# Optimization experiments

Measured on AMD Instinct MI355X. Metric: run time of the kernel, lower is better.

## Reference

```python
import jax, jax.numpy as jnp
import numpy as np
import itertools

G = 80          # voxel grid side
N = 200000      # active voxels
A, B = 64, 128  # in/out channels
K = 27          # 3x3x3 kernel offsets
EPS = 1e-5


def _build_kernel_map():
    rng = np.random.default_rng(0)
    flat = rng.choice(G ** 3, size=N, replace=False)
    coords = np.stack(np.unravel_index(flat, (G, G, G)), axis=1).astype(np.int64)  # [N,3]
    lookup = np.full(G ** 3, -1, dtype=np.int64)
    lookup[flat] = np.arange(N)
    gidx = np.full((K, N), N, dtype=np.int32)  # pad with dummy row N
    sidx = np.full((K, N), N, dtype=np.int32)
    for k, off in enumerate(itertools.product([-1, 0, 1], repeat=3)):
        nb = coords + np.asarray(off)
        valid = np.all((nb >= 0) & (nb < G), axis=1)
        i_all = np.nonzero(valid)[0]
        nbf = np.ravel_multi_index(nb[valid].T, (G, G, G))
        j = lookup[nbf]
        m = j >= 0
        i, j = i_all[m], j[m]
        e = len(i)
        gidx[k, :e] = j   # gather neighbor features
        sidx[k, :e] = i   # scatter to output voxel
    return jnp.asarray(gidx), jnp.asarray(sidx)


def setup_inputs() -> dict:
    key = jax.random.key(0)
    ks = jax.random.split(key, 8)
    gidx, sidx = _build_kernel_map()
    return {
        "feats": jax.random.normal(ks[0], (N, A), jnp.float32),
        "w1": jax.random.normal(ks[1], (K, A, B), jnp.float32) * (1.0 / np.sqrt(K * A)),
        "w2": jax.random.normal(ks[2], (K, B, B), jnp.float32) * (1.0 / np.sqrt(K * B)),
        "w_nin": jax.random.normal(ks[3], (A, B), jnp.float32) * (1.0 / np.sqrt(A)),
        "bn1_gamma": jnp.ones((A,), jnp.float32),
        "bn1_beta": jnp.zeros((A,), jnp.float32),
        "bn2_gamma": jnp.ones((B,), jnp.float32),
        "bn2_beta": jnp.zeros((B,), jnp.float32),
        "gidx": gidx,
        "sidx": sidx,
    }


def _bn(x, gamma, beta):
    # MinkowskiBatchNorm: per-channel stats over all active voxels (training mode)
    mean = jnp.mean(x, axis=0)
    var = jnp.var(x, axis=0)
    return (x - mean) * jax.lax.rsqrt(var + EPS) * gamma + beta


def _sparse_conv(feats, w, gidx, sidx):
    # Minkowski sparse conv: for each kernel offset k, gather neighbor feats,
    # apply W[k], scatter-add to output voxel. Dummy row N absorbs padding.
    fp = jnp.concatenate([feats, jnp.zeros((1, feats.shape[1]), feats.dtype)], axis=0)
    out = jnp.zeros((N + 1, w.shape[-1]), feats.dtype)
    for k in range(w.shape[0]):  # fixed 27 offsets
        out = out.at[sidx[k]].add(fp[gidx[k]] @ w[k])
    return out[:N]


def reference(feats, w1, w2, w_nin, bn1_gamma, bn1_beta, bn2_gamma, bn2_beta, gidx, sidx):
    # resblock: BN(a) -> conv3(a->b) -> BN(b) -> conv3(b->b); skip via 1x1 conv (a!=b)
    h = _bn(feats, bn1_gamma, bn1_beta)
    h = _sparse_conv(h, w1, gidx, sidx)
    h = _bn(h, bn2_gamma, bn2_beta)
    residual = _sparse_conv(h, w2, gidx, sidx)
    skip = feats @ w_nin  # kernel_size=1 conv == per-voxel linear
    return skip + residual
```

## Files before the change

kernel.cpp:

```cpp
#include <hip/hip_runtime.h>

#define N_VOX 200000
#define NPAD_INV (27 * N_VOX + 128)
#define EPS_BN 1e-5f

typedef __bf16 bf16x8 __attribute__((ext_vector_type(8)));
typedef float f32x4 __attribute__((ext_vector_type(4)));

__device__ __forceinline__ float bf2f(unsigned short u) {
    union { float f; unsigned int i; } x; x.i = ((unsigned int)u) << 16; return x.f;
}
__device__ __forceinline__ unsigned short f2bf(float f) {
    union { float f; unsigned int i; } x; x.f = f;
    unsigned int r = x.i + 0x7fffu + ((x.i >> 16) & 1u);
    return (unsigned short)(r >> 16);
}

#define ASYNC16(gsrc, ldst)                                                             \
    __builtin_amdgcn_global_load_lds(                                                   \
        (const __attribute__((address_space(1))) void*)(gsrc),                          \
        (__attribute__((address_space(3))) void*)(ldst), 16, 0, 0)

__global__ void fill_inv_kernel(int* __restrict__ inv) {
    for (int i = blockIdx.x * 256 + threadIdx.x; i < NPAD_INV; i += gridDim.x * 256)
        inv[i] = N_VOX;
}

__global__ void build_inv_kernel(const int* __restrict__ sidx, const int* __restrict__ gidx,
                                 int* __restrict__ inv) {
    int k = blockIdx.y;
    int p = blockIdx.x * 256 + threadIdx.x;
    if (p < N_VOX) {
        int s = sidx[k * N_VOX + p];
        if (s < N_VOX) inv[k * N_VOX + s] = gidx[k * N_VOX + p];
    }
}

__global__ void tr_w1_kernel(const float* __restrict__ w, unsigned short* __restrict__ wt) {
    int k = blockIdx.y; int idx = blockIdx.x * 256 + threadIdx.x;
    int a = idx >> 7, b = idx & 127;
    wt[k * 8192 + b * 64 + a] = f2bf(w[k * 8192 + idx]);
}
__global__ void tr_w2_kernel(const float* __restrict__ w, unsigned short* __restrict__ wt) {
    int k = blockIdx.y; int idx = blockIdx.x * 256 + threadIdx.x;
    int a = idx >> 7, b = idx & 127;
    wt[k * 16384 + b * 128 + a] = f2bf(w[k * 16384 + idx]);
}
__global__ void tr_wn_kernel(const float* __restrict__ w, unsigned short* __restrict__ wt) {
    int idx = blockIdx.x * 256 + threadIdx.x;
    int a = idx >> 7, b = idx & 127;
    wt[b * 64 + a] = f2bf(w[idx]);
}

__global__ void stats1_kernel(const float* __restrict__ feats,
                              float* __restrict__ sum, float* __restrict__ sq) {
    int t = threadIdx.x; int c = t & 63; int rg = t >> 6;
    float s = 0.f, q = 0.f;
    for (int row = blockIdx.x * 4 + rg; row < N_VOX; row += gridDim.x * 4) {
        float x = feats[(size_t)row * 64 + c];
        s += x; q += x * x;
    }
    __shared__ float red[8][64];
    red[rg][c] = s; red[4 + rg][c] = q;
    __syncthreads();
    if (t < 64) atomicAdd(&sum[t], red[0][t] + red[1][t] + red[2][t] + red[3][t]);
    else if (t < 128) { int cc = t - 64; atomicAdd(&sq[cc], red[4][cc] + red[5][cc] + red[6][cc] + red[7][cc]); }
}

__global__ void stats2_kernel(const unsigned short* __restrict__ h1b,
                              float* __restrict__ sum, float* __restrict__ sq) {
    int t = threadIdx.x; int c = t & 127; int rg = t >> 7;
    float s = 0.f, q = 0.f;
    for (int row = blockIdx.x * 2 + rg; row < N_VOX; row += gridDim.x * 2) {
        float x = bf2f(h1b[(size_t)row * 128 + c]);
        s += x; q += x * x;
    }
    __shared__ float red[4][128];
    red[rg][c] = s; red[2 + rg][c] = q;
    __syncthreads();
    if (t < 128) atomicAdd(&sum[t], red[0][t] + red[1][t]);
    else { int cc = t - 128; atomicAdd(&sq[cc], red[2][cc] + red[3][cc]); }
}

__global__ void norm1_kernel(const float* __restrict__ feats, const float* __restrict__ ssum,
                             const float* __restrict__ ssq, const float* __restrict__ gamma,
                             const float* __restrict__ beta, unsigned short* __restrict__ fA,
                             unsigned short* __restrict__ fRaw) {
    __shared__ float sc[64], sh[64];
    int t = threadIdx.x;
    if (t < 64) {
        float mean = ssum[t] * (1.0f / N_VOX);
        float var  = ssq[t] * (1.0f / N_VOX) - mean * mean;
        float s    = gamma[t] * rsqrtf(var + EPS_BN);
        sc[t] = s; sh[t] = beta[t] - mean * s;
    }
    __syncthreads();
    const int total = N_VOX * 64 / 8;
    int i = blockIdx.x * 256 + t;
    if (i >= total) return;
    int cb = (i * 8) & 63;
    const float4* src = (const float4*)(feats + (size_t)i * 8);
    float4 f0 = src[0], f1 = src[1];
    float fv[8] = {f0.x, f0.y, f0.z, f0.w, f1.x, f1.y, f1.z, f1.w};
    union { uint4 q; unsigned short u[8]; } a, r;
#pragma unroll
    for (int j = 0; j < 8; j++) {
        a.u[j] = f2bf(fv[j] * sc[cb + j] + sh[cb + j]);
        r.u[j] = f2bf(fv[j]);
    }
    *(uint4*)(fA + (size_t)i * 8) = a.q;
    *(uint4*)(fRaw + (size_t)i * 8) = r.q;
}

__global__ void norm2_kernel(unsigned short* __restrict__ h1b, const float* __restrict__ ssum,
                             const float* __restrict__ ssq, const float* __restrict__ gamma,
                             const float* __restrict__ beta) {
    __shared__ float sc[128], sh[128];
    int t = threadIdx.x;
    if (t < 128) {
        float mean = ssum[t] * (1.0f / N_VOX);
        float var  = ssq[t] * (1.0f / N_VOX) - mean * mean;
        float s    = gamma[t] * rsqrtf(var + EPS_BN);
        sc[t] = s; sh[t] = beta[t] - mean * s;
    }
    __syncthreads();
    const int total = N_VOX * 128 / 8;
    int i = blockIdx.x * 256 + t;
    if (i >= total) return;
    int cb = (i * 8) & 127;
    union { uint4 q; unsigned short u[8]; } v;
    v.q = *(const uint4*)(h1b + (size_t)i * 8);
#pragma unroll
    for (int j = 0; j < 8; j++) v.u[j] = f2bf(bf2f(v.u[j]) * sc[cb + j] + sh[cb + j]);
    *(uint4*)(h1b + (size_t)i * 8) = v.q;
}

__global__ __launch_bounds__(256) void conv1_kernel(
    const unsigned short* __restrict__ fA, const unsigned short* __restrict__ w1t,
    const int* __restrict__ inv, const unsigned short* __restrict__ zp,
    unsigned short* __restrict__ h1b) {
    __shared__ __align__(16) unsigned short sA[128 * 64];
    __shared__ __align__(16) unsigned short sB[128 * 64];
    const int t = threadIdx.x, lane = t & 63, w = t >> 6;
    const int v0 = blockIdx.x * 128;
    const int srow = w * 32;
    const int lrow = lane >> 3;
    const int lcol = (lane & 7) * 8;
    const int scol = lcol ^ (lrow * 8);
    const int m0 = (w & 1) * 64, n0 = (w >> 1) * 64;
    const int l16 = lane & 15, quad = lane >> 4;
    const int xs = l16 & 7;
    f32x4 acc[4][4] = {};

    for (int k = 0; k < 27; k++) {
#pragma unroll
        for (int q = 0; q < 4; q++) {
            int rt = srow + q * 8 + lrow;
            int g = inv[k * N_VOX + v0 + rt];
            const unsigned short* asrc = (g < N_VOX) ? (fA + (size_t)g * 64 + scol) : (zp + scol);
            ASYNC16(asrc, &sA[(srow + q * 8) * 64]);
            const unsigned short* bsrc = w1t + k * 8192 + rt * 64 + scol;
            ASYNC16(bsrc, &sB[(srow + q * 8) * 64]);
        }
        __syncthreads();
#pragma unroll
        for (int ks = 0; ks < 2; ks++) {
            const int cs = ((ks * 4 + quad) ^ xs) * 8;
            bf16x8 af[4], bfr[4];
#pragma unroll
            for (int mi = 0; mi < 4; mi++)
                af[mi] = *(const bf16x8*)&sA[(m0 + mi * 16 + l16) * 64 + cs];
#pragma unroll
            for (int ni = 0; ni < 4; ni++)
                bfr[ni] = *(const bf16x8*)&sB[(n0 + ni * 16 + l16) * 64 + cs];
#pragma unroll
            for (int mi = 0; mi < 4; mi++)
#pragma unroll
                for (int ni = 0; ni < 4; ni++)
                    acc[mi][ni] = __builtin_amdgcn_mfma_f32_16x16x32_bf16(af[mi], bfr[ni], acc[mi][ni], 0, 0, 0);
        }
        __syncthreads();
    }
#pragma unroll
    for (int mi = 0; mi < 4; mi++)
#pragma unroll
        for (int r = 0; r < 4; r++) {
            int v = v0 + m0 + mi * 16 + quad * 4 + r;
            if (v < N_VOX) {
#pragma unroll
                for (int ni = 0; ni < 4; ni++)
                    h1b[(size_t)v * 128 + n0 + ni * 16 + l16] = f2bf(acc[mi][ni][r]);
            }
        }
}

__global__ __launch_bounds__(256) void conv2_kernel(
    const unsigned short* __restrict__ h1n, const unsigned short* __restrict__ fRaw,
    const unsigned short* __restrict__ w2t, const unsigned short* __restrict__ w_nint,
    const int* __restrict__ inv, const unsigned short* __restrict__ zp,
    float* __restrict__ out) {
    __shared__ __align__(16) unsigned short sA[128 * 64];
    __shared__ __align__(16) unsigned short sB[128 * 64];
    const int t = threadIdx.x, lane = t & 63, w = t >> 6;
    const int v0 = blockIdx.x * 128;
    const int srow = w * 32;
    const int lrow = lane >> 3;
    const int lcol = (lane & 7) * 8;
    const int scol = lcol ^ (lrow * 8);
    const int m0 = (w & 1) * 64, n0 = (w >> 1) * 64;
    const int l16 = lane & 15, quad = lane >> 4;
    const int xs = l16 & 7;
    f32x4 acc[4][4] = {};

    for (int jj = 0; jj < 55; jj++) {
        if (jj < 54) {
            const int ko = jj >> 1;
            const int kh = (jj & 1) * 64;
#pragma unroll
            for (int q = 0; q < 4; q++) {
                int rt = srow + q * 8 + lrow;
                int g = inv[ko * N_VOX + v0 + rt];
                const unsigned short* asrc = (g < N_VOX) ? (h1n + (size_t)g * 128 + kh + scol) : (zp + scol);
                ASYNC16(asrc, &sA[(srow + q * 8) * 64]);
                const unsigned short* bsrc = w2t + ko * 16384 + rt * 128 + kh + scol;
                ASYNC16(bsrc, &sB[(srow + q * 8) * 64]);
            }
        } else {
#pragma unroll
            for (int q = 0; q < 4; q++) {
                int rt = srow + q * 8 + lrow;
                int v = v0 + rt;
                const unsigned short* asrc = (v < N_VOX) ? (fRaw + (size_t)v * 64 + scol) : (zp + scol);
                ASYNC16(asrc, &sA[(srow + q * 8) * 64]);
                const unsigned short* bsrc = w_nint + rt * 64 + scol;
                ASYNC16(bsrc, &sB[(srow + q * 8) * 64]);
            }
        }
        __syncthreads();
#pragma unroll
        for (int ks = 0; ks < 2; ks++) {
            const int cs = ((ks * 4 + quad) ^ xs) * 8;
            bf16x8 af[4], bfr[4];
#pragma unroll
            for (int mi = 0; mi < 4; mi++)
                af[mi] = *(const bf16x8*)&sA[(m0 + mi * 16 + l16) * 64 + cs];
#pragma unroll
            for (int ni = 0; ni < 4; ni++)
                bfr[ni] = *(const bf16x8*)&sB[(n0 + ni * 16 + l16) * 64 + cs];
#pragma unroll
            for (int mi = 0; mi < 4; mi++)
#pragma unroll
                for (int ni = 0; ni < 4; ni++)
                    acc[mi][ni] = __builtin_amdgcn_mfma_f32_16x16x32_bf16(af[mi], bfr[ni], acc[mi][ni], 0, 0, 0);
        }
        __syncthreads();
    }
#pragma unroll
    for (int mi = 0; mi < 4; mi++)
#pragma unroll
        for (int r = 0; r < 4; r++) {
            int v = v0 + m0 + mi * 16 + quad * 4 + r;
            if (v < N_VOX) {
#pragma unroll
                for (int ni = 0; ni < 4; ni++)
                    out[(size_t)v * 128 + n0 + ni * 16 + l16] = acc[mi][ni][r];
            }
        }
}

extern "C" void kernel_launch(void* const* d_in, const int* in_sizes, int n_in,
                              void* d_out, int out_size, void* d_ws, size_t ws_size,
                              hipStream_t stream) {
    const float* feats = (const float*)d_in[0];
    const float* w1    = (const float*)d_in[1];
    const float* w2    = (const float*)d_in[2];
    const float* w_nin = (const float*)d_in[3];
    const float* g1    = (const float*)d_in[4];
    const float* b1    = (const float*)d_in[5];
    const float* g2    = (const float*)d_in[6];
    const float* b2    = (const float*)d_in[7];
    const int* gidx = (const int*)d_in[8];
    const int* sidx = (const int*)d_in[9];
    float* out = (float*)d_out;

    char* ws = (char*)d_ws;
    int* inv               = (int*)(ws);
    unsigned short* fA     = (unsigned short*)(ws + 21600512);
    unsigned short* fRaw   = (unsigned short*)(ws + 47200512);
    unsigned short* h1b    = (unsigned short*)(ws + 72800512);
    unsigned short* w1t    = (unsigned short*)(ws + 124000512);
    unsigned short* w2t    = (unsigned short*)(ws + 124442880);
    unsigned short* w_nint = (unsigned short*)(ws + 125327616);
    float* stats           = (float*)(ws + 125344000);
    unsigned short* zp     = (unsigned short*)(ws + 125345536);
    float* s1sum = stats, *s1sq = stats + 64, *s2sum = stats + 128, *s2sq = stats + 256;

    hipMemsetAsync(stats, 0, 1536 + 256, stream);
    fill_inv_kernel<<<2048, 256, 0, stream>>>(inv);
    build_inv_kernel<<<dim3(782, 27), 256, 0, stream>>>(sidx, gidx, inv);
    tr_w1_kernel<<<dim3(32, 27), 256, 0, stream>>>(w1, w1t);
    tr_w2_kernel<<<dim3(64, 27), 256, 0, stream>>>(w2, w2t);
    tr_wn_kernel<<<32, 256, 0, stream>>>(w_nin, w_nint);
    stats1_kernel<<<512, 256, 0, stream>>>(feats, s1sum, s1sq);
    norm1_kernel<<<6250, 256, 0, stream>>>(feats, s1sum, s1sq, g1, b1, fA, fRaw);
    conv1_kernel<<<1563, 256, 0, stream>>>(fA, w1t, inv, zp, h1b);
    stats2_kernel<<<512, 256, 0, stream>>>(h1b, s2sum, s2sq);
    norm2_kernel<<<12500, 256, 0, stream>>>(h1b, s2sum, s2sq, g2, b2);
    conv2_kernel<<<1563, 256, 0, stream>>>(h1b, fRaw, w2t, w_nint, inv, zp, out);
}
```

Before: 816.2 us.

## Double-buffer LDS tiles in sparse conv kernels to overlap gather with MFMA

Both sparse conv kernels now hold two LDS buffers for the A and B tiles. Each loop step issues the async global-to-LDS loads for the next offset, then waits only on the previous loads with an explicit vmcnt count before computing. The aim is to hide the latency of the gathered neighbour rows behind MFMA work, and s_setprio raises wave priority during the MFMA burst. LDS use doubles to 64KB per block, which may cut occupancy, and correctness depends on the hand-written vmcnt(8) matching the number of loads issued per stage.

New measurement: 757.1 us. 1.08x faster.

```diff
diff --git a/kernel.cpp b/kernel.cpp
--- a/kernel.cpp
+++ b/kernel.cpp
@@ -139,8 +139,8 @@
     const unsigned short* __restrict__ fA, const unsigned short* __restrict__ w1t,
     const int* __restrict__ inv, const unsigned short* __restrict__ zp,
     unsigned short* __restrict__ h1b) {
-    __shared__ __align__(16) unsigned short sA[128 * 64];
-    __shared__ __align__(16) unsigned short sB[128 * 64];
+    __shared__ __align__(16) unsigned short sA[2][128 * 64];
+    __shared__ __align__(16) unsigned short sB[2][128 * 64];
     const int t = threadIdx.x, lane = t & 63, w = t >> 6;
     const int v0 = blockIdx.x * 128;
     const int srow = w * 32;
@@ -152,34 +152,51 @@
     const int xs = l16 & 7;
     f32x4 acc[4][4] = {};
 
-    for (int k = 0; k < 27; k++) {
+    auto stage = [&](int k, int b) {
 #pragma unroll
         for (int q = 0; q < 4; q++) {
             int rt = srow + q * 8 + lrow;
             int g = inv[k * N_VOX + v0 + rt];
             const unsigned short* asrc = (g < N_VOX) ? (fA + (size_t)g * 64 + scol) : (zp + scol);
-            ASYNC16(asrc, &sA[(srow + q * 8) * 64]);
+            ASYNC16(asrc, &sA[b][(srow + q * 8) * 64]);
             const unsigned short* bsrc = w1t + k * 8192 + rt * 64 + scol;
-            ASYNC16(bsrc, &sB[(srow + q * 8) * 64]);
-        }
-        __syncthreads();
+            ASYNC16(bsrc, &sB[b][(srow + q * 8) * 64]);
+        }
+    };
+
+    stage(0, 0);
+    for (int j = 0; j < 27; j++) {
+        const int cb = j & 1;
+        if (j + 1 < 27) {
+            stage(j + 1, cb ^ 1);
+            asm volatile("s_waitcnt vmcnt(8)" ::: "memory");
+        } else {
+            asm volatile("s_waitcnt vmcnt(0)" ::: "memory");
+        }
+        __builtin_amdgcn_sched_barrier(0);
+        __builtin_amdgcn_s_barrier();
+        __builtin_amdgcn_sched_barrier(0);
 #pragma unroll
         for (int ks = 0; ks < 2; ks++) {
             const int cs = ((ks * 4 + quad) ^ xs) * 8;
             bf16x8 af[4], bfr[4];
 #pragma unroll
             for (int mi = 0; mi < 4; mi++)
-                af[mi] = *(const bf16x8*)&sA[(m0 + mi * 16 + l16) * 64 + cs];
+                af[mi] = *(const bf16x8*)&sA[cb][(m0 + mi * 16 + l16) * 64 + cs];
 #pragma unroll
             for (int ni = 0; ni < 4; ni++)
-                bfr[ni] = *(const bf16x8*)&sB[(n0 + ni * 16 + l16) * 64 + cs];
+                bfr[ni] = *(const bf16x8*)&sB[cb][(n0 + ni * 16 + l16) * 64 + cs];
+            __builtin_amdgcn_s_setprio(1);
 #pragma unroll
             for (int mi = 0; mi < 4; mi++)
 #pragma unroll
                 for (int ni = 0; ni < 4; ni++)
                     acc[mi][ni] = __builtin_amdgcn_mfma_f32_16x16x32_bf16(af[mi], bfr[ni], acc[mi][ni], 0, 0, 0);
-        }
-        __syncthreads();
+            __builtin_amdgcn_s_setprio(0);
+        }
+        __builtin_amdgcn_sched_barrier(0);
+        __builtin_amdgcn_s_barrier();
+        __builtin_amdgcn_sched_barrier(0);
     }
 #pragma unroll
     for (int mi = 0; mi < 4; mi++)
@@ -199,8 +216,8 @@
     const unsigned short* __restrict__ w2t, const unsigned short* __restrict__ w_nint,
     const int* __restrict__ inv, const unsigned short* __restrict__ zp,
     float* __restrict__ out) {
-    __shared__ __align__(16) unsigned short sA[128 * 64];
-    __shared__ __align__(16) unsigned short sB[128 * 64];
+    __shared__ __align__(16) unsigned short sA[2][128 * 64];
+    __shared__ __align__(16) unsigned short sB[2][128 * 64];
     const int t = threadIdx.x, lane = t & 63, w = t >> 6;
     const int v0 = blockIdx.x * 128;
     const int srow = w * 32;
@@ -212,18 +229,18 @@
     const int xs = l16 & 7;
     f32x4 acc[4][4] = {};
 
-    for (int jj = 0; jj < 55; jj++) {
-        if (jj < 54) {
-            const int ko = jj >> 1;
-            const int kh = (jj & 1) * 64;
+    auto stage = [&](int j, int b) {
+        if (j < 54) {
+            const int ko = j >> 1;
+            const int kh = (j & 1) * 64;
 #pragma unroll
             for (int q = 0; q < 4; q++) {
                 int rt = srow + q * 8 + lrow;
                 int g = inv[ko * N_VOX + v0 + rt];
                 const unsigned short* asrc = (g < N_VOX) ? (h1n + (size_t)g * 128 + kh + scol) : (zp + scol);
-                ASYNC16(asrc, &sA[(srow + q * 8) * 64]);
+                ASYNC16(asrc, &sA[b][(srow + q * 8) * 64]);
                 const unsigned short* bsrc = w2t + ko * 16384 + rt * 128 + kh + scol;
-                ASYNC16(bsrc, &sB[(srow + q * 8) * 64]);
+                ASYNC16(bsrc, &sB[b][(srow + q * 8) * 64]);
             }
         } else {
 #pragma unroll
@@ -231,29 +248,46 @@
                 int rt = srow + q * 8 + lrow;
                 int v = v0 + rt;
                 const unsigned short* asrc = (v < N_VOX) ? (fRaw + (size_t)v * 64 + scol) : (zp + scol);
-                ASYNC16(asrc, &sA[(srow + q * 8) * 64]);
+                ASYNC16(asrc, &sA[b][(srow + q * 8) * 64]);
                 const unsigned short* bsrc = w_nint + rt * 64 + scol;
-                ASYNC16(bsrc, &sB[(srow + q * 8) * 64]);
+                ASYNC16(bsrc, &sB[b][(srow + q * 8) * 64]);
             }
         }
-        __syncthreads();
+    };
+
+    stage(0, 0);
+    for (int jj = 0; jj < 55; jj++) {
+        const int cb = jj & 1;
+        if (jj + 1 < 55) {
+            stage(jj + 1, cb ^ 1);
+            asm volatile("s_waitcnt vmcnt(8)" ::: "memory");
+        } else {
+            asm volatile("s_waitcnt vmcnt(0)" ::: "memory");
+        }
+        __builtin_amdgcn_sched_barrier(0);
+        __builtin_amdgcn_s_barrier();
+        __builtin_amdgcn_sched_barrier(0);
 #pragma unroll
         for (int ks = 0; ks < 2; ks++) {
             const int cs = ((ks * 4 + quad) ^ xs) * 8;
             bf16x8 af[4], bfr[4];
 #pragma unroll
             for (int mi = 0; mi < 4; mi++)
-                af[mi] = *(const bf16x8*)&sA[(m0 + mi * 16 + l16) * 64 + cs];
+                af[mi] = *(const bf16x8*)&sA[cb][(m0 + mi * 16 + l16) * 64 + cs];
 #pragma unroll
             for (int ni = 0; ni < 4; ni++)
-                bfr[ni] = *(const bf16x8*)&sB[(n0 + ni * 16 + l16) * 64 + cs];
+                bfr[ni] = *(const bf16x8*)&sB[cb][(n0 + ni * 16 + l16) * 64 + cs];
+            __builtin_amdgcn_s_setprio(1);
 #pragma unroll
             for (int mi = 0; mi < 4; mi++)
 #pragma unroll
                 for (int ni = 0; ni < 4; ni++)
                     acc[mi][ni] = __builtin_amdgcn_mfma_f32_16x16x32_bf16(af[mi], bfr[ni], acc[mi][ni], 0, 0, 0);
-        }
-        __syncthreads();
+            __builtin_amdgcn_s_setprio(0);
+        }
+        __builtin_amdgcn_sched_barrier(0);
+        __builtin_amdgcn_s_barrier();
+        __builtin_amdgcn_sched_barrier(0);
     }
 #pragma unroll
     for (int mi = 0; mi < 4; mi++)
```

## Pipeline conv gathers with 4-stage LDS ring and register-resident weights

Applied to the files above, without the earlier changes.

Both sparse conv kernels now run 512 threads (8 waves) per block. Each wave computes a 64x32 output tile. Weight tiles are loaded straight into registers, double-buffered across iterations, so they no longer go through LDS. Gathered neighbor rows are staged into a four-deep LDS ring with async loads issued two iterations ahead. A single barrier per step is guarded by explicit vmcnt waits, and MFMA priority is raised, all aimed at hiding gather latency behind compute. In exchange, each wave reloads weights from global/L2, LDS use rises to 64KB per block, and correctness depends on the hand-tuned waitcnt counts.

Measured after the change: 959.5 us. +17.6%, slower.

```diff
diff --git a/kernel.cpp b/kernel.cpp
--- a/kernel.cpp
+++ b/kernel.cpp
@@ -135,52 +135,81 @@
     *(uint4*)(h1b + (size_t)i * 8) = v.q;
 }
 
-__global__ __launch_bounds__(256) void conv1_kernel(
+
+#define CONV_ITER(J, BC, BN, NT)                                                        \
+    {                                                                                   \
+        if ((J) + 1 < (NT)) loadB((J) + 1, BN);                                         \
+        if ((J) + 2 < (NT)) stageA((J) + 2, ((J) + 2) & 3);                             \
+        __builtin_amdgcn_sched_barrier(0);                                              \
+        if ((J) + 2 < (NT))      asm volatile("s_waitcnt vmcnt(8)" ::: "memory");       \
+        else if ((J) + 1 < (NT)) asm volatile("s_waitcnt vmcnt(6)" ::: "memory");       \
+        else                     asm volatile("s_waitcnt vmcnt(0)" ::: "memory");       \
+        __builtin_amdgcn_sched_barrier(0);                                              \
+        __builtin_amdgcn_s_barrier();                                                   \
+        __builtin_amdgcn_sched_barrier(0);                                              \
+        compute((J) & 3, BC);                                                           \
+        __builtin_amdgcn_sched_barrier(0);                                              \
+    }
+
+__global__ __launch_bounds__(512, 4) void conv1_kernel(
     const unsigned short* __restrict__ fA, const unsigned short* __restrict__ w1t,
     const int* __restrict__ inv, const unsigned short* __restrict__ zp,
     unsigned short* __restrict__ h1b) {
-    __shared__ __align__(16) unsigned short sA[128 * 64];
-    __shared__ __align__(16) unsigned short sB[128 * 64];
+    __shared__ __align__(16) unsigned short sA[4][128 * 64];
     const int t = threadIdx.x, lane = t & 63, w = t >> 6;
     const int v0 = blockIdx.x * 128;
-    const int srow = w * 32;
     const int lrow = lane >> 3;
-    const int lcol = (lane & 7) * 8;
-    const int scol = lcol ^ (lrow * 8);
-    const int m0 = (w & 1) * 64, n0 = (w >> 1) * 64;
+    const int scol = ((lane & 7) * 8) ^ (lrow * 8);
+    const int wr = w & 1, wc = w >> 1;
+    const int m0 = wr * 64, n0 = wc * 32;
     const int l16 = lane & 15, quad = lane >> 4;
     const int xs = l16 & 7;
-    f32x4 acc[4][4] = {};
-
-    for (int k = 0; k < 27; k++) {
-#pragma unroll
-        for (int q = 0; q < 4; q++) {
-            int rt = srow + q * 8 + lrow;
+    f32x4 acc[4][2] = {};
+    bf16x8 br0[4], br1[4];
+
+    auto stageA = [&](int k, int b) {
+#pragma unroll
+        for (int q = 0; q < 2; q++) {
+            int rt = w * 16 + q * 8 + lrow;
             int g = inv[k * N_VOX + v0 + rt];
             const unsigned short* asrc = (g < N_VOX) ? (fA + (size_t)g * 64 + scol) : (zp + scol);
-            ASYNC16(asrc, &sA[(srow + q * 8) * 64]);
-            const unsigned short* bsrc = w1t + k * 8192 + rt * 64 + scol;
-            ASYNC16(bsrc, &sB[(srow + q * 8) * 64]);
-        }
-        __syncthreads();
+            ASYNC16(asrc, &sA[b][(w * 16 + q * 8) * 64]);
+        }
+    };
+    auto loadB = [&](int k, bf16x8* br) {
+        const unsigned short* base = w1t + k * 8192;
+#pragma unroll
+        for (int ni = 0; ni < 2; ni++)
+#pragma unroll
+            for (int ks = 0; ks < 2; ks++)
+                br[ni * 2 + ks] = *(const bf16x8*)(base + (n0 + ni * 16 + l16) * 64 + ks * 32 + quad * 8);
+    };
+    auto compute = [&](int b, const bf16x8* br) {
 #pragma unroll
         for (int ks = 0; ks < 2; ks++) {
             const int cs = ((ks * 4 + quad) ^ xs) * 8;
-            bf16x8 af[4], bfr[4];
+            bf16x8 af[4];
 #pragma unroll
             for (int mi = 0; mi < 4; mi++)
-                af[mi] = *(const bf16x8*)&sA[(m0 + mi * 16 + l16) * 64 + cs];
-#pragma unroll
-            for (int ni = 0; ni < 4; ni++)
-                bfr[ni] = *(const bf16x8*)&sB[(n0 + ni * 16 + l16) * 64 + cs];
+                af[mi] = *(const bf16x8*)&sA[b][(m0 + mi * 16 + l16) * 64 + cs];
+            __builtin_amdgcn_s_setprio(1);
 #pragma unroll
             for (int mi = 0; mi < 4; mi++)
 #pragma unroll
-                for (int ni = 0; ni < 4; ni++)
-                    acc[mi][ni] = __builtin_amdgcn_mfma_f32_16x16x32_bf16(af[mi], bfr[ni], acc[mi][ni], 0, 0, 0);
-        }
-        __syncthreads();
-    }
+                for (int ni = 0; ni < 2; ni++)
+                    acc[mi][ni] = __builtin_amdgcn_mfma_f32_16x16x32_bf16(af[mi], br[ni * 2 + ks], acc[mi][ni], 0, 0, 0);
+            __builtin_amdgcn_s_setprio(0);
+        }
+    };
+
+    stageA(0, 0); loadB(0, br0); stageA(1, 1);
+    int j = 0;
+    for (; j + 1 < 27; j += 2) {
+        CONV_ITER(j,     br0, br1, 27);
+        CONV_ITER(j + 1, br1, br0, 27);
+    }
+    CONV_ITER(26, br0, br1, 27);
+
 #pragma unroll
     for (int mi = 0; mi < 4; mi++)
 #pragma unroll
@@ -188,73 +217,92 @@
             int v = v0 + m0 + mi * 16 + quad * 4 + r;
             if (v < N_VOX) {
 #pragma unroll
-                for (int ni = 0; ni < 4; ni++)
+                for (int ni = 0; ni < 2; ni++)
                     h1b[(size_t)v * 128 + n0 + ni * 16 + l16] = f2bf(acc[mi][ni][r]);
             }
         }
 }
 
-__global__ __launch_bounds__(256) void conv2_kernel(
+__global__ __launch_bounds__(512, 4) void conv2_kernel(
     const unsigned short* __restrict__ h1n, const unsigned short* __restrict__ fRaw,
     const unsigned short* __restrict__ w2t, const unsigned short* __restrict__ w_nint,
     const int* __restrict__ inv, const unsigned short* __restrict__ zp,
     float* __restrict__ out) {
-    __shared__ __align__(16) unsigned short sA[128 * 64];
-    __shared__ __align__(16) unsigned short sB[128 * 64];
+    __shared__ __align__(16) unsigned short sA[4][128 * 64];
     const int t = threadIdx.x, lane = t & 63, w = t >> 6;
     const int v0 = blockIdx.x * 128;
-    const int srow = w * 32;
     const int lrow = lane >> 3;
-    const int lcol = (lane & 7) * 8;
-    const int scol = lcol ^ (lrow * 8);
-    const int m0 = (w & 1) * 64, n0 = (w >> 1) * 64;
+    const int scol = ((lane & 7) * 8) ^ (lrow * 8);
+    const int wr = w & 1, wc = w >> 1;
+    const int m0 = wr * 64, n0 = wc * 32;
     const int l16 = lane & 15, quad = lane >> 4;
     const int xs = l16 & 7;
-    f32x4 acc[4][4] = {};
-
-    for (int jj = 0; jj < 55; jj++) {
-        if (jj < 54) {
-            const int ko = jj >> 1;
-            const int kh = (jj & 1) * 64;
-#pragma unroll
-            for (int q = 0; q < 4; q++) {
-                int rt = srow + q * 8 + lrow;
+    f32x4 acc[4][2] = {};
+    bf16x8 br0[4], br1[4];
+
+    auto stageA = [&](int j, int b) {
+        if (j < 54) {
+            const int ko = j >> 1;
+            const int kh = (j & 1) * 64;
+#pragma unroll
+            for (int q = 0; q < 2; q++) {
+                int rt = w * 16 + q * 8 + lrow;
                 int g = inv[ko * N_VOX + v0 + rt];
                 const unsigned short* asrc = (g < N_VOX) ? (h1n + (size_t)g * 128 + kh + scol) : (zp + scol);
-                ASYNC16(asrc, &sA[(srow + q * 8) * 64]);
-                const unsigned short* bsrc = w2t + ko * 16384 + rt * 128 + kh + scol;
-                ASYNC16(bsrc, &sB[(srow + q * 8) * 64]);
+                ASYNC16(asrc, &sA[b][(w * 16 + q * 8) * 64]);
             }
         } else {
 #pragma unroll
-            for (int q = 0; q < 4; q++) {
-                int rt = srow + q * 8 + lrow;
+            for (int q = 0; q < 2; q++) {
+                int rt = w * 16 + q * 8 + lrow;
                 int v = v0 + rt;
                 const unsigned short* asrc = (v < N_VOX) ? (fRaw + (size_t)v * 64 + scol) : (zp + scol);
-                ASYNC16(asrc, &sA[(srow + q * 8) * 64]);
-                const unsigned short* bsrc = w_nint + rt * 64 + scol;
-                ASYNC16(bsrc, &sB[(srow + q * 8) * 64]);
+                ASYNC16(asrc, &sA[b][(w * 16 + q * 8) * 64]);
             }
         }
-        __syncthreads();
+    };
+    auto loadB = [&](int j, bf16x8* br) {
+        if (j < 54) {
+            const unsigned short* base = w2t + (j >> 1) * 16384 + (j & 1) * 64;
+#pragma unroll
+            for (int ni = 0; ni < 2; ni++)
+#pragma unroll
+                for (int ks = 0; ks < 2; ks++)
+                    br[ni * 2 + ks] = *(const bf16x8*)(base + (n0 + ni * 16 + l16) * 128 + ks * 32 + quad * 8);
+        } else {
+#pragma unroll
+            for (int ni = 0; ni < 2; ni++)
+#pragma unroll
+                for (int ks = 0; ks < 2; ks++)
+                    br[ni * 2 + ks] = *(const bf16x8*)(w_nint + (n0 + ni * 16 + l16) * 64 + ks * 32 + quad * 8);
+        }
+    };
+    auto compute = [&](int b, const bf16x8* br) {
 #pragma unroll
         for (int ks = 0; ks < 2; ks++) {
             const int cs = ((ks * 4 + quad) ^ xs) * 8;
-            bf16x8 af[4], bfr[4];
+            bf16x8 af[4];
 #pragma unroll
             for (int mi = 0; mi < 4; mi++)
-                af[mi] = *(const bf16x8*)&sA[(m0 + mi * 16 + l16) * 64 + cs];
-#pragma unroll
-            for (int ni = 0; ni < 4; ni++)
-                bfr[ni] = *(const bf16x8*)&sB[(n0 + ni * 16 + l16) * 64 + cs];
+                af[mi] = *(const bf16x8*)&sA[b][(m0 + mi * 16 + l16) * 64 + cs];
+            __builtin_amdgcn_s_setprio(1);
 #pragma unroll
             for (int mi = 0; mi < 4; mi++)
 #pragma unroll
-                for (int ni = 0; ni < 4; ni++)
-                    acc[mi][ni] = __builtin_amdgcn_mfma_f32_16x16x32_bf16(af[mi], bfr[ni], acc[mi][ni], 0, 0, 0);
-        }
-        __syncthreads();
-    }
+                for (int ni = 0; ni < 2; ni++)
+                    acc[mi][ni] = __builtin_amdgcn_mfma_f32_16x16x32_bf16(af[mi], br[ni * 2 + ks], acc[mi][ni], 0, 0, 0);
+            __builtin_amdgcn_s_setprio(0);
+        }
+    };
+
+    stageA(0, 0); loadB(0, br0); stageA(1, 1);
+    int j = 0;
+    for (; j + 1 < 55; j += 2) {
+        CONV_ITER(j,     br0, br1, 55);
+        CONV_ITER(j + 1, br1, br0, 55);
+    }
+    CONV_ITER(54, br0, br1, 55);
+
 #pragma unroll
     for (int mi = 0; mi < 4; mi++)
 #pragma unroll
@@ -262,7 +310,7 @@
             int v = v0 + m0 + mi * 16 + quad * 4 + r;
             if (v < N_VOX) {
 #pragma unroll
-                for (int ni = 0; ni < 4; ni++)
+                for (int ni = 0; ni < 2; ni++)
                     out[(size_t)v * 128 + n0 + ni * 16 + l16] = acc[mi][ni][r];
             }
         }
@@ -303,8 +351,8 @@
     tr_wn_kernel<<<32, 256, 0, stream>>>(w_nin, w_nint);
     stats1_kernel<<<512, 256, 0, stream>>>(feats, s1sum, s1sq);
     norm1_kernel<<<6250, 256, 0, stream>>>(feats, s1sum, s1sq, g1, b1, fA, fRaw);
-    conv1_kernel<<<1563, 256, 0, stream>>>(fA, w1t, inv, zp, h1b);
+    conv1_kernel<<<1563, 512, 0, stream>>>(fA, w1t, inv, zp, h1b);
     stats2_kernel<<<512, 256, 0, stream>>>(h1b, s2sum, s2sq);
     norm2_kernel<<<12500, 256, 0, stream>>>(h1b, s2sum, s2sq, g2, b2);
-    conv2_kernel<<<1563, 256, 0, stream>>>(h1b, fRaw, w2t, w_nint, inv, zp, out);
-}
+    conv2_kernel<<<1563, 512, 0, stream>>>(h1b, fRaw, w2t, w_nint, inv, zp, out);
+}
```
